# Kernel optimization log

Measured on AMD Instinct MI355X. Metric: run time of the kernel, lower is better.

The kernel has to match this reference:

```python
import jax, jax.numpy as jnp
import numpy as np

# res_scale = (max(scale)+float_scale)/max(scale) = 2.5/2 = 1.25
RES_SCALE = 1.25


def _dct(x):
    # DCT-II via FFT (Makhoul), norm=None, matching torch module's dct().
    # x: [..., N]
    N = x.shape[-1]
    v = jnp.concatenate([x[..., ::2], x[..., 1::2][..., ::-1]], axis=-1)
    Vc = jnp.fft.fft(v, axis=-1)  # full FFT == _rfft(onesided=False)
    k = -jnp.arange(N, dtype=x.dtype) * (np.pi / (2.0 * N))
    V = 2.0 * (Vc.real * jnp.cos(k) - Vc.imag * jnp.sin(k))
    return V.astype(x.dtype)


def _idct(X):
    # Inverse of DCT-II (norm=None), matching torch module's idct().
    # X: [..., N]
    N = X.shape[-1]
    Xv = X / 2.0
    k = jnp.arange(N, dtype=X.dtype) * (np.pi / (2.0 * N))
    Wr, Wi = jnp.cos(k), jnp.sin(k)
    Vt_r = Xv
    Vt_i = jnp.concatenate([jnp.zeros_like(Xv[..., :1]), -Xv[..., ::-1][..., :-1]], axis=-1)
    V_r = Vt_r * Wr - Vt_i * Wi
    V_i = Vt_r * Wi + Vt_i * Wr
    # _irfft(onesided=False): keep first N//2+1 bins, irfft back to length N
    Vc = (V_r[..., : N // 2 + 1] + 1j * V_i[..., : N // 2 + 1]).astype(jnp.complex64)
    v = jnp.fft.irfft(Vc, n=N, axis=-1).astype(X.dtype)
    # odd/even de-shuffle
    x = jnp.zeros_like(v)
    x = x.at[..., ::2].set(v[..., : N - N // 2])
    x = x.at[..., 1::2].set(v[..., ::-1][..., : N // 2])
    return x


def _dct_2d(x):
    return jnp.swapaxes(_dct(jnp.swapaxes(_dct(x), -1, -2)), -1, -2)


def _idct_2d(X):
    return jnp.swapaxes(_idct(jnp.swapaxes(_idct(X), -1, -2)), -1, -2)


def setup_inputs() -> dict:
    key = jax.random.key(0)
    x = jax.random.normal(key, (16, 3, 768, 768), dtype=jnp.float32)
    return {"x": x}


def reference(x):
    B, C, H, W = x.shape
    outH, outW = int(H * RES_SCALE), int(W * RES_SCALE)
    X = _dct_2d(x)
    # ZeroPad2d((0, outW-W, 0, outH-H)): pad right and bottom with zeros
    X = jnp.pad(X, ((0, 0), (0, 0), (0, outH - H), (0, outW - W)))
    return _idct_2d(X)
```

## Files before the change

### kernel.cpp

```cpp
#include <hip/hip_runtime.h>


#define HW 768
#define OHW 960
#define NIMG 48

typedef __attribute__((ext_vector_type(8))) short short8;
typedef __attribute__((ext_vector_type(4))) float f32x4;
typedef __attribute__((ext_vector_type(4))) float float4v;
typedef __attribute__((ext_vector_type(4))) unsigned short us4;

__device__ __forceinline__ unsigned short f2bf(float f) {
    union { float f; unsigned int u; } v; v.f = f;
    unsigned int u = v.u;
    return (unsigned short)((u + 0x7FFFu + ((u >> 16) & 1u)) >> 16);
}

__device__ __forceinline__ void glds16(const void* g, void* l) {
    __builtin_amdgcn_global_load_lds(
        (const __attribute__((address_space(1))) void*)g,
        (__attribute__((address_space(3))) void*)l, 16, 0, 0);
}

__device__ __forceinline__ float dsum(int p) {
    int n1 = (767 * p) % 30720;
    int n2 = (768 * p) % 30720;
    const float w = (float)(3.14159265358979323846 / 15360.0);
    return sinf((float)n1 * w) * cosf((float)n2 * w) / sinf((float)p * w);
}

__global__ void fill_M(unsigned short* __restrict__ Mb) {
    int idx = blockIdx.x * 256 + threadIdx.x;
    if (idx >= OHW * HW) return;
    int i = idx / HW, n = idx - i * HW;
    int a = 8 * i + 4, b = 10 * n + 5;
    int p1 = a + b;
    int p2 = a - b; if (p2 < 0) p2 += 15360;
    float m = (1.0f + dsum(p1) + dsum(p2)) * (1.0f / 960.0f);
    Mb[idx] = f2bf(m);
}

__global__ void conv_bf16(const float* __restrict__ x, unsigned short* __restrict__ xb, int n4) {
    int i = blockIdx.x * 256 + threadIdx.x;
    if (i >= n4) return;
    float4v v = *(const float4v*)(x + (size_t)i * 4);
    us4 o; o.x = f2bf(v.x); o.y = f2bf(v.y); o.z = f2bf(v.z); o.w = f2bf(v.w);
    *(us4*)(xb + (size_t)i * 4) = o;
}

__global__ __launch_bounds__(256) void gemm_bt(
    const unsigned short* __restrict__ A, int lda,
    const unsigned short* __restrict__ Bg, long long strideB, int ldb,
    void* __restrict__ Cg, long long strideC, int ldc,
    int Md, int Nd, int Kd, int out_f32)
{
    __shared__ unsigned short As[2][128 * 64];
    __shared__ unsigned short Bs[2][128 * 64];

    const int tid = threadIdx.x;
    const int wave = tid >> 6, lane = tid & 63;
    const int wm = wave >> 1, wn = wave & 1;
    const int t16 = lane & 15, quad = lane >> 4;
    const int z = blockIdx.z;

    const unsigned short* Bp = Bg + (size_t)z * strideB;
    const int mb = blockIdx.y * 128, nbb = blockIdx.x * 128;

    f32x4 acc[4][4];
#pragma unroll
    for (int i = 0; i < 4; ++i)
#pragma unroll
        for (int j = 0; j < 4; ++j)
            acc[i][j] = (f32x4){0.f, 0.f, 0.f, 0.f};

    const int srow = tid >> 3;
    const int klog = (((tid & 7) ^ ((tid >> 4) & 7))) * 8;
    const unsigned short* pA[4];
    const unsigned short* pB[4];
#pragma unroll
    for (int j = 0; j < 4; ++j) {
        int ra = mb + srow + 32 * j;  if (ra >= Md) ra = Md - 1;
        int rb = nbb + srow + 32 * j; if (rb >= Nd) rb = Nd - 1;
        pA[j] = A  + (size_t)ra * lda + klog;
        pB[j] = Bp + (size_t)rb * ldb + klog;
    }
    unsigned short* dA = &As[0][0] + tid * 8;
    unsigned short* dB = &Bs[0][0] + tid * 8;

    const int swz = (t16 >> 1) & 7;
    int aOff[2], bOff[2];
#pragma unroll
    for (int ks = 0; ks < 2; ++ks) {
        int ph = ((ks * 4 + quad) ^ swz) * 8;
        aOff[ks] = (wm * 64 + t16) * 64 + ph;
        bOff[ks] = (wn * 64 + t16) * 64 + ph;
    }

#define STAGE(buf, kt) do {                                                   \
    int kk_ = (kt) * 64;                                                      \
    _Pragma("unroll")                                                         \
    for (int j_ = 0; j_ < 4; ++j_)                                            \
        glds16(pA[j_] + kk_, dA + (buf) * 8192 + j_ * 2048);                  \
    _Pragma("unroll")                                                         \
    for (int j_ = 0; j_ < 4; ++j_)                                            \
        glds16(pB[j_] + kk_, dB + (buf) * 8192 + j_ * 2048);                  \
} while (0)

#define COMPUTE(buf) do {                                                     \
    _Pragma("unroll")                                                         \
    for (int ks_ = 0; ks_ < 2; ++ks_) {                                       \
        short8 af_[4], bf_[4];                                                \
        _Pragma("unroll")                                                     \
        for (int mi_ = 0; mi_ < 4; ++mi_)                                     \
            af_[mi_] = *(const short8*)(&As[buf][0] + aOff[ks_] + mi_ * 1024);\
        _Pragma("unroll")                                                     \
        for (int ni_ = 0; ni_ < 4; ++ni_)                                     \
            bf_[ni_] = *(const short8*)(&Bs[buf][0] + bOff[ks_] + ni_ * 1024);\
        _Pragma("unroll")                                                     \
        for (int mi_ = 0; mi_ < 4; ++mi_)                                     \
        _Pragma("unroll")                                                     \
        for (int ni_ = 0; ni_ < 4; ++ni_)                                     \
            acc[mi_][ni_] = __builtin_amdgcn_mfma_f32_16x16x32_bf16(          \
                af_[mi_], bf_[ni_], acc[mi_][ni_], 0, 0, 0);                  \
    }                                                                         \
} while (0)

    const int NT = Kd >> 6;

    STAGE(0, 0);
    __syncthreads();

    for (int kt = 0; kt + 2 <= NT; kt += 2) {
        STAGE(1, kt + 1);
        COMPUTE(0);
        __syncthreads();
        if (kt + 2 < NT) STAGE(0, kt + 2);
        COMPUTE(1);
        __syncthreads();
    }

#undef STAGE
#undef COMPUTE

    const int gr0 = mb + wm * 64;
    const int gc0 = nbb + wn * 64;
    if (out_f32) {
        float* C = (float*)Cg + (size_t)z * strideC;
#pragma unroll
        for (int mi = 0; mi < 4; ++mi)
#pragma unroll
            for (int ni = 0; ni < 4; ++ni) {
                int col = gc0 + ni * 16 + t16;
                if (col < Nd) {
#pragma unroll
                    for (int r = 0; r < 4; ++r) {
                        int rowg = gr0 + mi * 16 + quad * 4 + r;
                        if (rowg < Md) C[(size_t)rowg * ldc + col] = acc[mi][ni][r];
                    }
                }
            }
    } else {
        unsigned short* C = (unsigned short*)Cg + (size_t)z * strideC;
#pragma unroll
        for (int mi = 0; mi < 4; ++mi)
#pragma unroll
            for (int ni = 0; ni < 4; ++ni) {
                int col = gc0 + ni * 16 + t16;
                if (col < Nd) {
#pragma unroll
                    for (int r = 0; r < 4; ++r) {
                        int rowg = gr0 + mi * 16 + quad * 4 + r;
                        if (rowg < Md) C[(size_t)rowg * ldc + col] = f2bf(acc[mi][ni][r]);
                    }
                }
            }
    }
}

extern "C" void kernel_launch(void* const* d_in, const int* in_sizes, int n_in,
                              void* d_out, int out_size, void* d_ws, size_t ws_size,
                              hipStream_t stream) {
    const float* x = (const float*)d_in[0];
    float* out = (float*)d_out;
    char* ws = (char*)d_ws;

    size_t offM  = 0;
    size_t fixed = offM + (size_t)OHW * HW * 2;
    size_t perImg = (size_t)HW * HW * 2 + (size_t)OHW * HW * 2;

    int nb = 1;
    if (ws_size > fixed + perImg) {
        size_t q = (ws_size - fixed) / perImg;
        nb = (q > 48) ? 48 : (int)q;
        if (nb < 1) nb = 1;
    }

    unsigned short* Mb = (unsigned short*)(ws + offM);
    unsigned short* xb = (unsigned short*)(ws + fixed);
    unsigned short* T  = (unsigned short*)(ws + fixed + (size_t)nb * HW * HW * 2);

    fill_M<<<(OHW * HW + 255) / 256, 256, 0, stream>>>(Mb);

    for (int b0 = 0; b0 < NIMG; b0 += nb) {
        int cur = NIMG - b0; if (cur > nb) cur = nb;
        int n4 = cur * (HW * HW / 4);
        conv_bf16<<<(n4 + 255) / 256, 256, 0, stream>>>(
            x + (size_t)b0 * HW * HW, xb, n4);
        gemm_bt<<<dim3(6, 8, cur), 256, 0, stream>>>(
            Mb, HW, xb, (long long)HW * HW, HW,
            T, (long long)OHW * HW, HW, OHW, HW, HW, 0);
        gemm_bt<<<dim3(8, 8, cur), 256, 0, stream>>>(
            Mb, HW, T, (long long)OHW * HW, HW,
            out + (size_t)b0 * OHW * OHW, (long long)OHW * OHW, OHW,
            OHW, OHW, HW, 1);
    }
    (void)in_sizes; (void)n_in; (void)out_size;
}
```

Measured before the change: 419.9 us.

## Enlarge GEMM tiles to 256x256 with 8-wave phased MFMA/LDS pipeline

The batched bf16 GEMM kernel moves from 128x128 tiles with 4 waves to 256x256 tiles with 8 waves, each wave computing 128x64. The K loop is split into four MMA quarter phases, with explicit waitcnt and barrier control and raised wave priority during MFMA. Global-to-LDS prefetch of the next tile is interleaved with these phases. The aim is more data reuse per LDS byte and better overlap of loads with matrix math. The cost is 128KB of LDS per block, which limits occupancy, plus extra padded work on the 960-sized dimension.

New measurement: 413.6 us. No clear change (-1.5%).

```diff
diff --git a/kernel.cpp b/kernel.cpp
--- a/kernel.cpp
+++ b/kernel.cpp
@@ -48,106 +48,140 @@
     *(us4*)(xb + (size_t)i * 4) = o;
 }
 
-__global__ __launch_bounds__(256) void gemm_bt(
+#define ASM_BAR   asm volatile("s_barrier" ::: "memory")
+#define ASM_VM0   asm volatile("s_waitcnt vmcnt(0)" ::: "memory")
+#define ASM_LGKM8 asm volatile("s_waitcnt lgkmcnt(8)" ::: "memory")
+#define ASM_LGKM0 do { asm volatile("s_waitcnt lgkmcnt(0)" ::: "memory"); \
+                       __builtin_amdgcn_sched_barrier(0); } while (0)
+
+__global__ __launch_bounds__(512, 2) void gemm_bt(
     const unsigned short* __restrict__ A, int lda,
     const unsigned short* __restrict__ Bg, long long strideB, int ldb,
     void* __restrict__ Cg, long long strideC, int ldc,
     int Md, int Nd, int Kd, int out_f32)
 {
-    __shared__ unsigned short As[2][128 * 64];
-    __shared__ unsigned short Bs[2][128 * 64];
+    __shared__ unsigned short As[2][256 * 64];
+    __shared__ unsigned short Bs[2][256 * 64];
 
     const int tid = threadIdx.x;
     const int wave = tid >> 6, lane = tid & 63;
-    const int wm = wave >> 1, wn = wave & 1;
+    const int wm = wave >> 2, wn = wave & 3;
     const int t16 = lane & 15, quad = lane >> 4;
     const int z = blockIdx.z;
 
     const unsigned short* Bp = Bg + (size_t)z * strideB;
-    const int mb = blockIdx.y * 128, nbb = blockIdx.x * 128;
-
-    f32x4 acc[4][4];
-#pragma unroll
-    for (int i = 0; i < 4; ++i)
+    const int mb = blockIdx.y * 256, nbb = blockIdx.x * 256;
+
+    f32x4 acc[8][4];
+#pragma unroll
+    for (int i = 0; i < 8; ++i)
 #pragma unroll
         for (int j = 0; j < 4; ++j)
             acc[i][j] = (f32x4){0.f, 0.f, 0.f, 0.f};
 
     const int srow = tid >> 3;
-    const int klog = (((tid & 7) ^ ((tid >> 4) & 7))) * 8;
+    const int klog = ((tid & 7) ^ ((tid >> 4) & 7)) * 8;
     const unsigned short* pA[4];
     const unsigned short* pB[4];
 #pragma unroll
     for (int j = 0; j < 4; ++j) {
-        int ra = mb + srow + 32 * j;  if (ra >= Md) ra = Md - 1;
-        int rb = nbb + srow + 32 * j; if (rb >= Nd) rb = Nd - 1;
+        int ra = mb + srow + 64 * j;  if (ra >= Md) ra = Md - 1;
+        int rb = nbb + srow + 64 * j; if (rb >= Nd) rb = Nd - 1;
         pA[j] = A  + (size_t)ra * lda + klog;
         pB[j] = Bp + (size_t)rb * ldb + klog;
     }
-    unsigned short* dA = &As[0][0] + tid * 8;
-    unsigned short* dB = &Bs[0][0] + tid * 8;
+    const int dOff = tid * 8;
 
     const int swz = (t16 >> 1) & 7;
-    int aOff[2], bOff[2];
-#pragma unroll
-    for (int ks = 0; ks < 2; ++ks) {
-        int ph = ((ks * 4 + quad) ^ swz) * 8;
-        aOff[ks] = (wm * 64 + t16) * 64 + ph;
-        bOff[ks] = (wn * 64 + t16) * 64 + ph;
-    }
-
-#define STAGE(buf, kt) do {                                                   \
-    int kk_ = (kt) * 64;                                                      \
+    const int ph0 = ((0 * 4 + quad) ^ swz) * 8;
+    const int ph1 = ((1 * 4 + quad) ^ swz) * 8;
+    const int aRow = (wm * 128 + t16) * 64;
+    const int bRow = (wn * 64 + t16) * 64;
+
+#define RD_A(mig) do { _Pragma("unroll")                                      \
+    for (int mi_ = 0; mi_ < 4; ++mi_) {                                       \
+        afr[mi_][0] = *(const short8*)(Asc + aRow + ((mig)*4+mi_)*1024 + ph0);\
+        afr[mi_][1] = *(const short8*)(Asc + aRow + ((mig)*4+mi_)*1024 + ph1);\
+    } } while (0)
+
+#define RD_B(dst, nig) do { _Pragma("unroll")                                 \
+    for (int ni_ = 0; ni_ < 2; ++ni_) {                                       \
+        dst[ni_][0] = *(const short8*)(Bsc + bRow + ((nig)*2+ni_)*1024 + ph0);\
+        dst[ni_][1] = *(const short8*)(Bsc + bRow + ((nig)*2+ni_)*1024 + ph1);\
+    } } while (0)
+
+#define MMA_Q(mig, nig, bfv) do {                                             \
+    __builtin_amdgcn_s_setprio(1);                                            \
     _Pragma("unroll")                                                         \
+    for (int ks_ = 0; ks_ < 2; ++ks_)                                         \
+    _Pragma("unroll")                                                         \
+    for (int mi_ = 0; mi_ < 4; ++mi_)                                         \
+    _Pragma("unroll")                                                         \
+    for (int ni_ = 0; ni_ < 2; ++ni_)                                         \
+        acc[(mig)*4+mi_][(nig)*2+ni_] =                                       \
+            __builtin_amdgcn_mfma_f32_16x16x32_bf16(                          \
+                afr[mi_][ks_], bfv[ni_][ks_],                                 \
+                acc[(mig)*4+mi_][(nig)*2+ni_], 0, 0, 0);                      \
+    __builtin_amdgcn_s_setprio(0); } while (0)
+
+#define STG_A(buf, kt) do { _Pragma("unroll")                                 \
     for (int j_ = 0; j_ < 4; ++j_)                                            \
-        glds16(pA[j_] + kk_, dA + (buf) * 8192 + j_ * 2048);                  \
-    _Pragma("unroll")                                                         \
+        glds16(pA[j_] + (kt) * 64, &As[buf][0] + dOff + j_ * 4096); } while (0)
+#define STG_B(buf, kt) do { _Pragma("unroll")                                 \
     for (int j_ = 0; j_ < 4; ++j_)                                            \
-        glds16(pB[j_] + kk_, dB + (buf) * 8192 + j_ * 2048);                  \
-} while (0)
-
-#define COMPUTE(buf) do {                                                     \
-    _Pragma("unroll")                                                         \
-    for (int ks_ = 0; ks_ < 2; ++ks_) {                                       \
-        short8 af_[4], bf_[4];                                                \
-        _Pragma("unroll")                                                     \
-        for (int mi_ = 0; mi_ < 4; ++mi_)                                     \
-            af_[mi_] = *(const short8*)(&As[buf][0] + aOff[ks_] + mi_ * 1024);\
-        _Pragma("unroll")                                                     \
-        for (int ni_ = 0; ni_ < 4; ++ni_)                                     \
-            bf_[ni_] = *(const short8*)(&Bs[buf][0] + bOff[ks_] + ni_ * 1024);\
-        _Pragma("unroll")                                                     \
-        for (int mi_ = 0; mi_ < 4; ++mi_)                                     \
-        _Pragma("unroll")                                                     \
-        for (int ni_ = 0; ni_ < 4; ++ni_)                                     \
-            acc[mi_][ni_] = __builtin_amdgcn_mfma_f32_16x16x32_bf16(          \
-                af_[mi_], bf_[ni_], acc[mi_][ni_], 0, 0, 0);                  \
-    }                                                                         \
-} while (0)
+        glds16(pB[j_] + (kt) * 64, &Bs[buf][0] + dOff + j_ * 4096); } while (0)
 
     const int NT = Kd >> 6;
 
-    STAGE(0, 0);
-    __syncthreads();
-
-    for (int kt = 0; kt + 2 <= NT; kt += 2) {
-        STAGE(1, kt + 1);
-        COMPUTE(0);
-        __syncthreads();
-        if (kt + 2 < NT) STAGE(0, kt + 2);
-        COMPUTE(1);
-        __syncthreads();
-    }
-
-#undef STAGE
-#undef COMPUTE
-
-    const int gr0 = mb + wm * 64;
+    STG_A(0, 0); STG_B(0, 0);
+    ASM_VM0;
+    ASM_BAR;
+
+    for (int t = 0; t < NT; ++t) {
+        const int cur = t & 1, nxt = cur ^ 1;
+        const unsigned short* Asc = &As[cur][0];
+        const unsigned short* Bsc = &Bs[cur][0];
+        const bool pf = (t + 1 < NT);
+        short8 afr[4][2], bf0[2][2], bf1[2][2];
+
+        RD_A(0); RD_B(bf0, 0);
+        if (pf) STG_A(nxt, t + 1);
+        ASM_LGKM8;
+        ASM_BAR;
+        ASM_LGKM0;
+        MMA_Q(0, 0, bf0);
+        ASM_BAR;
+
+        RD_B(bf1, 1);
+        if (pf) STG_B(nxt, t + 1);
+        ASM_BAR;
+        ASM_LGKM0;
+        MMA_Q(0, 1, bf1);
+        ASM_BAR;
+
+        RD_A(1);
+        ASM_BAR;
+        ASM_LGKM0;
+        MMA_Q(1, 0, bf0);
+        ASM_BAR;
+
+        MMA_Q(1, 1, bf1);
+        ASM_VM0;
+        ASM_BAR;
+    }
+
+#undef RD_A
+#undef RD_B
+#undef MMA_Q
+#undef STG_A
+#undef STG_B
+
+    const int gr0 = mb + wm * 128;
     const int gc0 = nbb + wn * 64;
     if (out_f32) {
         float* C = (float*)Cg + (size_t)z * strideC;
 #pragma unroll
-        for (int mi = 0; mi < 4; ++mi)
+        for (int mi = 0; mi < 8; ++mi)
 #pragma unroll
             for (int ni = 0; ni < 4; ++ni) {
                 int col = gc0 + ni * 16 + t16;
@@ -162,7 +196,7 @@
     } else {
         unsigned short* C = (unsigned short*)Cg + (size_t)z * strideC;
 #pragma unroll
-        for (int mi = 0; mi < 4; ++mi)
+        for (int mi = 0; mi < 8; ++mi)
 #pragma unroll
             for (int ni = 0; ni < 4; ++ni) {
                 int col = gc0 + ni * 16 + t16;
@@ -206,10 +240,10 @@
         int n4 = cur * (HW * HW / 4);
         conv_bf16<<<(n4 + 255) / 256, 256, 0, stream>>>(
             x + (size_t)b0 * HW * HW, xb, n4);
-        gemm_bt<<<dim3(6, 8, cur), 256, 0, stream>>>(
+        gemm_bt<<<dim3(3, 4, cur), 512, 0, stream>>>(
             Mb, HW, xb, (long long)HW * HW, HW,
             T, (long long)OHW * HW, HW, OHW, HW, HW, 0);
-        gemm_bt<<<dim3(8, 8, cur), 256, 0, stream>>>(
+        gemm_bt<<<dim3(4, 4, cur), 512, 0, stream>>>(
             Mb, HW, T, (long long)OHW * HW, HW,
             out + (size_t)b0 * OHW * OHW, (long long)OHW * OHW, OHW,
             OHW, OHW, HW, 1);
```
